# Kernel optimization log

Hardware: AMD Instinct MI355X
Metric: run time of the kernel (lower is better)

Reference implementation:

```python
import math
import jax, jax.numpy as jnp
import numpy as np

H = 8
DIM = 256
HD = DIM // H
SCALE = math.sqrt(HD)
EPS = 1e-16


def _segment_softmax(scores, dst, num_nodes):
    # scores: [E, H], dst: [E] -> softmax over edges sharing the same dst
    m = jax.ops.segment_max(scores, dst, num_segments=num_nodes)  # [N, H]
    m = jnp.where(jnp.isfinite(m), m, 0.0)  # empty segments -> -inf -> 0
    e = jnp.exp(scores - m[dst])
    s = jax.ops.segment_sum(e, dst, num_segments=num_nodes)  # [N, H]
    return e / (s[dst] + EPS)


def _graph_attention(x, edges, wq, bq, wk, bk, wv, bv, wo, bo):
    # x: [N, DIM]; edges: [2, E] (src, dst). Dropout is identity (eval mode).
    N = x.shape[0]
    Q = (x @ wq + bq).reshape(N, H, HD)
    K = (x @ wk + bk).reshape(N, H, HD)
    V = (x @ wv + bv).reshape(N, H, HD)
    src, dst = edges[0], edges[1]
    scores = jnp.einsum('ehd,ehd->eh', Q[dst], K[src]) / SCALE  # [E, H]
    attn = _segment_softmax(scores, dst, N)  # [E, H]
    msgs = V[src] * attn[:, :, None]  # [E, H, HD]
    out = jax.ops.segment_sum(msgs, dst, num_segments=N).reshape(N, DIM)
    return out @ wo + bo


def _linear_params(key, fan_in, fan_out):
    k1, k2 = jax.random.split(key)
    bound = 1.0 / math.sqrt(fan_in)
    w = jax.random.uniform(k1, (fan_in, fan_out), minval=-bound, maxval=bound, dtype=jnp.float32)
    b = jax.random.uniform(k2, (fan_out,), minval=-bound, maxval=bound, dtype=jnp.float32)
    return w, b


def setup_inputs() -> dict:
    key = jax.random.key(0)
    ks = jax.random.split(key, 12)
    n_slot, n_dom = 20000, 1000
    e_slot, e_dom = 320000, 16000
    inp = {
        'slot_x': jax.random.normal(ks[0], (n_slot, DIM), dtype=jnp.float32),
        'domain_x': jax.random.normal(ks[1], (n_dom, DIM), dtype=jnp.float32),
        'slot_edges': jax.random.randint(ks[2], (2, e_slot), 0, n_slot, dtype=jnp.int32),
        'domain_edges': jax.random.randint(ks[3], (2, e_dom), 0, n_dom, dtype=jnp.int32),
    }
    names = ['wq', 'wk', 'wv', 'wo']
    for i, nm in enumerate(names):
        w, b = _linear_params(ks[4 + i], DIM, DIM)
        inp[f'slot_{nm}'] = w
        inp[f'slot_{nm}_b'] = b
    for i, nm in enumerate(names):
        w, b = _linear_params(ks[8 + i], DIM, DIM)
        inp[f'dom_{nm}'] = w
        inp[f'dom_{nm}_b'] = b
    return inp


def reference(slot_x, domain_x, slot_edges, domain_edges,
              slot_wq, slot_wq_b, slot_wk, slot_wk_b, slot_wv, slot_wv_b, slot_wo, slot_wo_b,
              dom_wq, dom_wq_b, dom_wk, dom_wk_b, dom_wv, dom_wv_b, dom_wo, dom_wo_b):
    # slot branch: self-attention on slot graph + identity residual
    slot_out = _graph_attention(slot_x, slot_edges,
                                slot_wq, slot_wq_b, slot_wk, slot_wk_b,
                                slot_wv, slot_wv_b, slot_wo, slot_wo_b) + slot_x
    # domain branch
    dom_out = _graph_attention(domain_x, domain_edges,
                               dom_wq, dom_wq_b, dom_wk, dom_wk_b,
                               dom_wv, dom_wv_b, dom_wo, dom_wo_b) + domain_x
    return slot_out, dom_out
```

## Files before the change

### kernel.cpp

```cpp
#include <hip/hip_runtime.h>
#include <hip/hip_bf16.h>

#define DIM 256
#define INV_SCALE 0.17677669529663687f
#define SM_EPS 1e-16f
#define CAP 64
#define EPT 4

typedef unsigned short ushortT;
typedef unsigned int uintT;
typedef __attribute__((ext_vector_type(8))) __bf16 bf16x8;
typedef __attribute__((ext_vector_type(4))) float f32x4;

__device__ __forceinline__ float bf2f(ushortT u) {
    return __uint_as_float(((uintT)u) << 16);
}
__device__ __forceinline__ ushortT f2bf(float f) {
    uintT u = __float_as_uint(f);
    u += 0x7FFFu + ((u >> 16) & 1u);
    return (ushortT)(u >> 16);
}
template <int CTRL>
__device__ __forceinline__ float qperm_add(float p) {
    int v = __builtin_amdgcn_update_dpp(0, __float_as_int(p), CTRL, 0xF, 0xF, true);
    return p + __int_as_float(v);
}

struct WPack { const void* w[8]; const void* b[8]; };

__device__ __forceinline__ bool sniff_m16(const ushortT* __restrict__ x) {
    int lane = threadIdx.x & 63;
    ushortT u = x[lane * 2];
    int e = (u >> 7) & 0xFF;
    bool sane = ((u & 0x7FFFu) == 0) || (e >= 0x66 && e <= 0x90);
    unsigned long long m = __ballot(sane);
    return __popcll(m) >= 32;
}

__global__ __launch_bounds__(256) void megaA(
        const void* __restrict__ xs, const void* __restrict__ xd,
        const ushortT* __restrict__ sniff_src,
        ushortT* __restrict__ xb_s, ushortT* __restrict__ xb_d,
        WPack pk, ushortT* __restrict__ wT, float* __restrict__ biasF,
        int* __restrict__ flagWs,
        const int* __restrict__ src_s, const int* __restrict__ dst_s,
        const int* __restrict__ src_d, const int* __restrict__ dst_d,
        int* __restrict__ cnt_s, int* __restrict__ cnt_d,
        int* __restrict__ col_s, int* __restrict__ col_d,
        int Es_, int Ed_, int nSc,
        int n4s, int n4d, int nA0, int nA1)
{
    const int bid = blockIdx.x;
    const int t = threadIdx.x;

    if (bid < nSc) {
        const int base = bid * (256 * EPT) + t;
        #pragma unroll
        for (int u = 0; u < EPT; ++u) {
            const int idx = base + u * 256;
            if (idx < Es_) {
                const int dv = dst_s[idx];
                const int pos = atomicAdd(&cnt_s[dv], 1);
                if (pos < CAP) col_s[(dv << 6) + pos] = src_s[idx];
            } else {
                const int e = idx - Es_;
                if (e < Ed_) {
                    const int dv = dst_d[e];
                    const int pos = atomicAdd(&cnt_d[dv], 1);
                    if (pos < CAP) col_d[(dv << 6) + pos] = src_d[e];
                }
            }
        }
        return;
    }
    const bool m16 = sniff_m16(sniff_src);
    const int li2 = bid - nSc;

    if (li2 < nA0 + nA1) {
        const bool d = li2 >= nA0;
        const int li = d ? li2 - nA0 : li2;
        const int n4 = d ? n4d : n4s;
        const int i = li * 256 + t;
        if (i >= n4) return;
        const void* x = d ? xd : xs;
        ushortT* xb = d ? xb_d : xb_s;
        if (m16) {
            ((ushort4*)xb)[i] = ((const ushort4*)x)[i];
        } else {
            float4 v = ((const float4*)x)[i];
            ushort4 o2;
            o2.x = f2bf(v.x); o2.y = f2bf(v.y); o2.z = f2bf(v.z); o2.w = f2bf(v.w);
            ((ushort4*)xb)[i] = o2;
        }
    } else if (li2 < nA0 + nA1 + 128) {
        __shared__ float sh[64][65];
        const int r0 = li2 - (nA0 + nA1);
        const int which = r0 >> 4;
        const int tile = r0 & 15;
        const int tr = tile >> 2, tc = tile & 3;
        const void* w = pk.w[which];
        const int tx = t & 63, tg = t >> 6;
        #pragma unroll
        for (int i = 0; i < 16; ++i) {
            const int r = i * 4 + tg;
            const size_t si = (size_t)(tr * 64 + r) * 256 + tc * 64 + tx;
            sh[r][tx] = m16 ? bf2f(((const ushortT*)w)[si]) : ((const float*)w)[si];
        }
        __syncthreads();
        ushortT* o = wT + (size_t)which * 65536;
        #pragma unroll
        for (int i = 0; i < 16; ++i) {
            const int r = i * 4 + tg;
            o[(size_t)(tc * 64 + r) * 256 + tr * 64 + tx] = f2bf(sh[tx][r]);
        }
    } else if (li2 < nA0 + nA1 + 136) {
        const int which = li2 - (nA0 + nA1 + 128);
        const void* b = pk.b[which];
        float v = m16 ? bf2f(((const ushortT*)b)[t]) : ((const float*)b)[t];
        biasF[which * 256 + t] = v;
    } else {
        if (t == 0) *flagWs = m16 ? 1 : 0;
    }
}

__global__ __launch_bounds__(256, 2) void megaB(
        const ushortT* __restrict__ xb_s, const ushortT* __restrict__ xb_d,
        const ushortT* __restrict__ wT, const float* __restrict__ biasF,
        ushortT* __restrict__ q_s, ushortT* __restrict__ kv_s,
        ushortT* __restrict__ q_d, ushortT* __restrict__ kv_d,
        int Ms, int Md, int nbs_, int nbq_)
{
    const int bid = blockIdx.x;
    const int by  = bid / nbq_;
    const int bx0 = bid % nbq_;
    const bool dom = bx0 >= nbs_;
    const int bx = dom ? bx0 - nbs_ : bx0;
    const ushortT* A = dom ? xb_d : xb_s;
    const int M = dom ? Md : Ms;
    const int wbase = dom ? 4 : 0;
    ushortT* Q = dom ? q_d : q_s;
    ushortT* KV = dom ? kv_d : kv_s;

    __shared__ ushortT As[64 * 256];
    __shared__ ushortT Cs[3][64 * 70];

    const int tid  = threadIdx.x;
    const int wid  = tid >> 6;
    const int lane = tid & 63;
    const int m    = lane & 15;
    const int q    = lane >> 4;
    const int row0 = bx * 64;
    const int col0 = by * 64;
    const int colw = col0 + wid * 16 + m;

    {
        const int r  = tid >> 2;
        const int qt = tid & 3;
        const size_t rowAddr = (size_t)min(row0 + r, M - 1) * DIM;
        const int xr = r & 7;
        #pragma unroll
        for (int j = 0; j < 8; ++j) {
            const int chunk = qt * 8 + j;
            uint4 v = *(const uint4*)(A + rowAddr + chunk * 8);
            *(uint4*)&As[r * 256 + ((chunk ^ xr) * 8)] = v;
        }
    }

    const ushortT* Bp = wT + (size_t)wbase * 65536 + (size_t)colw * DIM + q * 8;
    bf16x8 bl[8][3];
    #pragma unroll
    for (int kk = 0; kk < 8; ++kk)
        #pragma unroll
        for (int z = 0; z < 3; ++z)
            bl[kk][z] = *(const bf16x8*)(Bp + (size_t)z * 65536 + kk * 32);

    f32x4 acc[3][4];
    #pragma unroll
    for (int z = 0; z < 3; ++z)
        #pragma unroll
        for (int i = 0; i < 4; ++i)
            acc[z][i] = (f32x4){0.f, 0.f, 0.f, 0.f};

    const int xm = m & 7;

    __syncthreads();

    #pragma unroll
    for (int kk = 0; kk < 8; ++kk) {
        bf16x8 af[4];
        #pragma unroll
        for (int i = 0; i < 4; ++i)
            af[i] = *(const bf16x8*)&As[(i * 16 + m) * 256 + (((q + 4 * kk) ^ xm) * 8)];
        #pragma unroll
        for (int z = 0; z < 3; ++z)
            #pragma unroll
            for (int i = 0; i < 4; ++i)
                acc[z][i] = __builtin_amdgcn_mfma_f32_16x16x32_bf16(bl[kk][z], af[i], acc[z][i], 0, 0, 0);
    }

    #pragma unroll
    for (int z = 0; z < 3; ++z) {
        const float4 b4 = *(const float4*)&biasF[(wbase + z) * 256 + col0 + wid * 16 + q * 4];
        #pragma unroll
        for (int i = 0; i < 4; ++i) {
            const int r = i * 16 + m;
            ushort4 o;
            o.x = f2bf(acc[z][i][0] + b4.x);
            o.y = f2bf(acc[z][i][1] + b4.y);
            o.z = f2bf(acc[z][i][2] + b4.z);
            o.w = f2bf(acc[z][i][3] + b4.w);
            *(ushort4*)&Cs[z][r * 70 + wid * 16 + q * 4] = o;
        }
    }
    __syncthreads();

    {
        const int r = tid >> 2;
        const int c = (tid & 3) * 16;
        const int row = row0 + r;
        if (row < M) {
            #pragma unroll
            for (int z = 0; z < 3; ++z) {
                uint4 v0 = *(const uint4*)&Cs[z][r * 70 + c];
                uint4 v1 = *(const uint4*)&Cs[z][r * 70 + c + 8];
                ushortT* C = (z == 0)
                    ? (Q + (size_t)row * DIM + col0 + c)
                    : (KV + (size_t)row * 512 + (z - 1) * 256 + col0 + c);
                *(uint4*)C = v0;
                *(uint4*)(C + 8) = v1;
            }
        }
    }
}

__global__ __launch_bounds__(256) void attn_kernel(
        const ushortT* __restrict__ Qs, const ushortT* __restrict__ KVs,
        const int* __restrict__ cnts, const int* __restrict__ css,
        ushortT* __restrict__ aggs,
        const ushortT* __restrict__ Qd_, const ushortT* __restrict__ KVd_,
        const int* __restrict__ cntd, const int* __restrict__ csd,
        ushortT* __restrict__ aggd,
        int Ns_, int Ntot)
{
    const int g = blockIdx.x * 4 + (threadIdx.x >> 6);
    if (g >= Ntot) return;
    const bool dom = g >= Ns_;
    const int d = dom ? g - Ns_ : g;
    const int t = threadIdx.x & 63;
    const ushortT* Qb = dom ? Qd_ : Qs;
    const ushortT* KVb = dom ? KVd_ : KVs;
    const int* cnt = dom ? cntd : cnts;
    const int* colsrc = dom ? csd : css;
    ushortT* aggb = dom ? aggd : aggs;

    const uintT t4 = (uintT)t * 4;
    const size_t cbase = (size_t)d * DIM + t4;
    uint2 qv = *(const uint2*)(Qb + cbase);
    const float q0 = bf2f((ushortT)(qv.x & 0xFFFF)), q1 = bf2f((ushortT)(qv.x >> 16));
    const float q2 = bf2f((ushortT)(qv.y & 0xFFFF)), q3 = bf2f((ushortT)(qv.y >> 16));

    float a0 = 0.f, a1 = 0.f, a2 = 0.f, a3 = 0.f, den = 0.f;

    auto PROC = [&](uint2 kvc, uint2 vvc) {
        float k0 = bf2f((ushortT)(kvc.x & 0xFFFF)), k1 = bf2f((ushortT)(kvc.x >> 16));
        float k2 = bf2f((ushortT)(kvc.y & 0xFFFF)), k3 = bf2f((ushortT)(kvc.y >> 16));
        float p = q0 * k0 + q1 * k1 + q2 * k2 + q3 * k3;
        p = qperm_add<0xB1>(p);
        p = qperm_add<0x4E>(p);
        p += __shfl_xor(p, 4, 8);
        const float w = __expf(fminf(p * INV_SCALE, 60.0f));
        den += w;
        a0 += w * bf2f((ushortT)(vvc.x & 0xFFFF));
        a1 += w * bf2f((ushortT)(vvc.x >> 16));
        a2 += w * bf2f((ushortT)(vvc.y & 0xFFFF));
        a3 += w * bf2f((ushortT)(vvc.y >> 16));
    };

    int deg = cnt[d];
    if (deg > CAP) deg = CAP;
    const int* cl = colsrc + ((size_t)d << 6);
    int i = 0;
    for (; i + 8 <= deg; i += 8) {
        const int4 c0 = *(const int4*)(cl + i);
        const int4 c1 = *(const int4*)(cl + i + 4);
        const uintT o0 = ((uintT)c0.x << 9) + t4;
        const uintT o1 = ((uintT)c0.y << 9) + t4;
        const uintT o2 = ((uintT)c0.z << 9) + t4;
        const uintT o3 = ((uintT)c0.w << 9) + t4;
        const uintT o4 = ((uintT)c1.x << 9) + t4;
        const uintT o5 = ((uintT)c1.y << 9) + t4;
        const uintT o6 = ((uintT)c1.z << 9) + t4;
        const uintT o7 = ((uintT)c1.w << 9) + t4;
        uint2 k0v = *(const uint2*)(KVb + o0), v0v = *(const uint2*)(KVb + o0 + 256);
        uint2 k1v = *(const uint2*)(KVb + o1), v1v = *(const uint2*)(KVb + o1 + 256);
        uint2 k2v = *(const uint2*)(KVb + o2), v2v = *(const uint2*)(KVb + o2 + 256);
        uint2 k3v = *(const uint2*)(KVb + o3), v3v = *(const uint2*)(KVb + o3 + 256);
        uint2 k4v = *(const uint2*)(KVb + o4), v4v = *(const uint2*)(KVb + o4 + 256);
        uint2 k5v = *(const uint2*)(KVb + o5), v5v = *(const uint2*)(KVb + o5 + 256);
        uint2 k6v = *(const uint2*)(KVb + o6), v6v = *(const uint2*)(KVb + o6 + 256);
        uint2 k7v = *(const uint2*)(KVb + o7), v7v = *(const uint2*)(KVb + o7 + 256);
        PROC(k0v, v0v); PROC(k1v, v1v); PROC(k2v, v2v); PROC(k3v, v3v);
        PROC(k4v, v4v); PROC(k5v, v5v); PROC(k6v, v6v); PROC(k7v, v7v);
    }
    for (; i + 4 <= deg; i += 4) {
        const int4 c0 = *(const int4*)(cl + i);
        const uintT o0 = ((uintT)c0.x << 9) + t4;
        const uintT o1 = ((uintT)c0.y << 9) + t4;
        const uintT o2 = ((uintT)c0.z << 9) + t4;
        const uintT o3 = ((uintT)c0.w << 9) + t4;
        uint2 k0v = *(const uint2*)(KVb + o0), v0v = *(const uint2*)(KVb + o0 + 256);
        uint2 k1v = *(const uint2*)(KVb + o1), v1v = *(const uint2*)(KVb + o1 + 256);
        uint2 k2v = *(const uint2*)(KVb + o2), v2v = *(const uint2*)(KVb + o2 + 256);
        uint2 k3v = *(const uint2*)(KVb + o3), v3v = *(const uint2*)(KVb + o3 + 256);
        PROC(k0v, v0v); PROC(k1v, v1v); PROC(k2v, v2v); PROC(k3v, v3v);
    }
    for (; i < deg; ++i) {
        const uintT sb = ((uintT)cl[i] << 9) + t4;
        uint2 kv = *(const uint2*)(KVb + sb);
        uint2 vv = *(const uint2*)(KVb + sb + 256);
        PROC(kv, vv);
    }

    const float r = 1.0f / (den + SM_EPS);
    ushort4 o;
    o.x = f2bf(a0 * r); o.y = f2bf(a1 * r); o.z = f2bf(a2 * r); o.w = f2bf(a3 * r);
    *(ushort4*)(aggb + cbase) = o;
}

__global__ __launch_bounds__(256, 2) void gemm_out(
        const ushortT* __restrict__ As_, const ushortT* __restrict__ Ad_,
        const ushortT* __restrict__ wT, const float* __restrict__ biasF,
        const void* __restrict__ xs, const void* __restrict__ xd,
        void* __restrict__ dout, int Ms, int Md, int nbs,
        const int* __restrict__ flag)
{
    const bool dom = (int)blockIdx.x >= nbs;
    const int bx = dom ? blockIdx.x - nbs : blockIdx.x;
    const ushortT* A = dom ? Ad_ : As_;
    const int M = dom ? Md : Ms;
    const int widx = 3 + (dom ? 4 : 0);
    const ushortT* BT = wT + (size_t)widx * 65536;
    const float* bias = biasF + widx * 256;
    const void* res = dom ? xd : xs;
    const size_t outOff = dom ? (size_t)Ms * DIM : 0;

    __shared__ ushortT As2[64 * 256];
    __shared__ float Cf[64 * 66];

    const int tid  = threadIdx.x;
    const int wid  = tid >> 6;
    const int lane = tid & 63;
    const int m    = lane & 15;
    const int q    = lane >> 4;
    const int row0 = bx * 64;
    const int col0 = blockIdx.y * 64;
    const int colw = col0 + wid * 16 + m;

    {
        const int r  = tid >> 2;
        const int qt = tid & 3;
        const size_t rowAddr = (size_t)min(row0 + r, M - 1) * DIM;
        const int xr = r & 7;
        #pragma unroll
        for (int j = 0; j < 8; ++j) {
            const int chunk = qt * 8 + j;
            uint4 v = *(const uint4*)(A + rowAddr + chunk * 8);
            *(uint4*)&As2[r * 256 + ((chunk ^ xr) * 8)] = v;
        }
    }

    const ushortT* Bp = BT + (size_t)colw * DIM + q * 8;
    bf16x8 bl[8];
    #pragma unroll
    for (int kk = 0; kk < 8; ++kk)
        bl[kk] = *(const bf16x8*)(Bp + kk * 32);

    f32x4 acc[4];
    #pragma unroll
    for (int i = 0; i < 4; ++i) acc[i] = (f32x4){0.f, 0.f, 0.f, 0.f};

    const int xm = m & 7;

    __syncthreads();

    #pragma unroll
    for (int kk = 0; kk < 8; ++kk) {
        bf16x8 af[4];
        #pragma unroll
        for (int i = 0; i < 4; ++i)
            af[i] = *(const bf16x8*)&As2[(i * 16 + m) * 256 + (((q + 4 * kk) ^ xm) * 8)];
        #pragma unroll
        for (int i = 0; i < 4; ++i)
            acc[i] = __builtin_amdgcn_mfma_f32_16x16x32_bf16(bl[kk], af[i], acc[i], 0, 0, 0);
    }

    {
        const float4 b4 = *(const float4*)&bias[col0 + wid * 16 + q * 4];
        #pragma unroll
        for (int i = 0; i < 4; ++i) {
            const int r = i * 16 + m;
            float4 o;
            o.x = acc[i][0] + b4.x;
            o.y = acc[i][1] + b4.y;
            o.z = acc[i][2] + b4.z;
            o.w = acc[i][3] + b4.w;
            *(float4*)&Cf[r * 66 + wid * 16 + q * 4] = o;
        }
    }
    __syncthreads();

    {
        const bool m16 = (*flag != 0);
        const int r = tid >> 2;
        const int c = (tid & 3) * 16;
        const int row = row0 + r;
        if (row < M) {
            const size_t ridx = (size_t)row * DIM + col0 + c;
            float v[16];
            #pragma unroll
            for (int j = 0; j < 16; j += 4) {
                float4 cv = *(const float4*)&Cf[r * 66 + c + j];
                v[j] = cv.x; v[j + 1] = cv.y; v[j + 2] = cv.z; v[j + 3] = cv.w;
            }
            if (m16) {
                const ushortT* rp = (const ushortT*)res + ridx;
                ushortT* op = (ushortT*)dout + outOff + ridx;
                uint4 r0 = *(const uint4*)rp;
                uint4 r1 = *(const uint4*)(rp + 8);
                ushortT tmp[16];
                const uintT* rw0 = (const uintT*)&r0;
                const uintT* rw1 = (const uintT*)&r1;
                #pragma unroll
                for (int j = 0; j < 4; ++j) {
                    tmp[2 * j]     = f2bf(v[2 * j]     + bf2f((ushortT)(rw0[j] & 0xFFFF)));
                    tmp[2 * j + 1] = f2bf(v[2 * j + 1] + bf2f((ushortT)(rw0[j] >> 16)));
                    tmp[8 + 2 * j]     = f2bf(v[8 + 2 * j]     + bf2f((ushortT)(rw1[j] & 0xFFFF)));
                    tmp[8 + 2 * j + 1] = f2bf(v[8 + 2 * j + 1] + bf2f((ushortT)(rw1[j] >> 16)));
                }
                *(uint4*)op = *(const uint4*)&tmp[0];
                *(uint4*)(op + 8) = *(const uint4*)&tmp[8];
            } else {
                const float* rp = (const float*)res + ridx;
                float* op = (float*)dout + outOff + ridx;
                #pragma unroll
                for (int j = 0; j < 16; j += 4) {
                    float4 rv = *(const float4*)(rp + j);
                    float4 o;
                    o.x = v[j] + rv.x; o.y = v[j + 1] + rv.y;
                    o.z = v[j + 2] + rv.z; o.w = v[j + 3] + rv.w;
                    *(float4*)(op + j) = o;
                }
            }
        }
    }
}

extern "C" void kernel_launch(void* const* d_in, const int* in_sizes, int n_in,
                              void* d_out, int out_size, void* d_ws, size_t ws_size,
                              hipStream_t stream)
{
    const void* slot_x = d_in[0];
    const void* dom_x  = d_in[1];
    const int* slot_edges = (const int*)d_in[2];
    const int* dom_edges  = (const int*)d_in[3];
    const int Ns = in_sizes[0] / DIM;
    const int Nd = in_sizes[1] / DIM;
    const int Es = in_sizes[2] / 2;
    const int Ed = in_sizes[3] / 2;

    WPack pk;
    for (int i = 0; i < 8; ++i) { pk.w[i] = d_in[4 + 2 * i]; pk.b[i] = d_in[5 + 2 * i]; }

    char* p = (char*)d_ws;
    size_t o = 0;
    auto take = [&](size_t b) { void* r = p + o; o = (o + b + 255) & ~(size_t)255; return r; };
    const size_t ndS = (size_t)Ns * DIM;
    const size_t ndD = (size_t)Nd * DIM;
    ushortT* xb_s  = (ushortT*)take(ndS * 2);
    ushortT* q_s   = (ushortT*)take(ndS * 2);
    ushortT* kv_s  = (ushortT*)take(2 * ndS * 2);
    ushortT* agg_s = (ushortT*)take(ndS * 2);
    ushortT* xb_d  = (ushortT*)take(ndD * 2);
    ushortT* q_d   = (ushortT*)take(ndD * 2);
    ushortT* kv_d  = (ushortT*)take(2 * ndD * 2);
    ushortT* agg_d = (ushortT*)take(ndD * 2);
    ushortT* wT    = (ushortT*)take(8 * 65536 * 2);
    float*   biasF = (float*)take(8 * 256 * 4);
    int* cnt_s = (int*)take((size_t)(Ns + Nd) * 4);
    int* cnt_d = cnt_s + Ns;
    int* col_s = (int*)take((size_t)Ns * CAP * 4);
    int* col_d = (int*)take((size_t)Nd * CAP * 4);
    int* flagWs = (int*)take(256);

    const int* src_s = slot_edges;
    const int* dst_s = slot_edges + Es;
    const int* src_d = dom_edges;
    const int* dst_d = dom_edges + Ed;

    const int n4s = Ns * DIM / 4, n4d = Nd * DIM / 4;
    const int nbs = (Ns + 63) / 64;
    const int nbd = (Nd + 63) / 64;
    const int nbq = nbs + nbd;

    (void)hipMemsetAsync(cnt_s, 0, (size_t)(Ns + Nd) * 4, stream);

    const int Etot = Es + Ed;
    const int nSc = (Etot + 256 * EPT - 1) / (256 * EPT);
    const int nA0 = (n4s + 255) / 256;
    const int nA1 = (n4d + 255) / 256;
    hipLaunchKernelGGL(megaA, dim3(nSc + nA0 + nA1 + 136 + 1), dim3(256), 0, stream,
                       slot_x, dom_x, (const ushortT*)slot_x, xb_s, xb_d,
                       pk, wT, biasF, flagWs,
                       src_s, dst_s, src_d, dst_d,
                       cnt_s, cnt_d, col_s, col_d,
                       Es, Ed, nSc, n4s, n4d, nA0, nA1);

    hipLaunchKernelGGL(megaB, dim3(nbq * 4), dim3(256), 0, stream,
                       xb_s, xb_d, wT, biasF, q_s, kv_s, q_d, kv_d,
                       Ns, Nd, nbs, nbq);

    const int Ntot = Ns + Nd;
    hipLaunchKernelGGL(attn_kernel, dim3((Ntot + 3) / 4), dim3(256), 0, stream,
                       q_s, kv_s, cnt_s, col_s, agg_s,
                       q_d, kv_d, cnt_d, col_d, agg_d,
                       Ns, Ntot);

    hipLaunchKernelGGL(gemm_out, dim3(nbq, DIM / 64), dim3(256), 0, stream,
                       agg_s, agg_d, wT, biasF, slot_x, dom_x, d_out,
                       Ns, Nd, nbs, flagWs);
}
```

Before: 222.1 us.

## Fuse x bf16 conversion into QKV GEMM and move edge scatter into it

Removes the separate pass that converts x to a bf16 staging buffer; the QKV GEMM now reads x directly and converts fp32 to bf16 while filling shared memory. Edge CSR scatter blocks move from the prep kernel into the GEMM kernel, so the prep kernel only transposes weights and biases. This saves a full read/write of x through the workspace and lets scatter overlap with the GEMM. The cost is that each GEMM column block re-reads fp32 x (four times as many blocks along columns), which doubles the load bytes per tile versus bf16.

```diff
diff --git a/kernel.cpp b/kernel.cpp
--- a/kernel.cpp
+++ b/kernel.cpp
@@ -38,23 +38,60 @@
 }
 
 __global__ __launch_bounds__(256) void megaA(
+        const ushortT* __restrict__ sniff_src,
+        WPack pk, ushortT* __restrict__ wT, float* __restrict__ biasF,
+        int* __restrict__ flagWs)
+{
+    const bool m16 = sniff_m16(sniff_src);
+    const int bid = blockIdx.x;
+    const int t = threadIdx.x;
+
+    if (bid < 128) {
+        __shared__ float sh[64][65];
+        const int which = bid >> 4;
+        const int tile = bid & 15;
+        const int tr = tile >> 2, tc = tile & 3;
+        const void* w = pk.w[which];
+        const int tx = t & 63, tg = t >> 6;
+        #pragma unroll
+        for (int i = 0; i < 16; ++i) {
+            const int r = i * 4 + tg;
+            const size_t si = (size_t)(tr * 64 + r) * 256 + tc * 64 + tx;
+            sh[r][tx] = m16 ? bf2f(((const ushortT*)w)[si]) : ((const float*)w)[si];
+        }
+        __syncthreads();
+        ushortT* o = wT + (size_t)which * 65536;
+        #pragma unroll
+        for (int i = 0; i < 16; ++i) {
+            const int r = i * 4 + tg;
+            o[(size_t)(tc * 64 + r) * 256 + tr * 64 + tx] = f2bf(sh[tx][r]);
+        }
+    } else if (bid < 136) {
+        const int which = bid - 128;
+        const void* b = pk.b[which];
+        float v = m16 ? bf2f(((const ushortT*)b)[t]) : ((const float*)b)[t];
+        biasF[which * 256 + t] = v;
+    } else {
+        if (t == 0) *flagWs = m16 ? 1 : 0;
+    }
+}
+
+__global__ __launch_bounds__(256, 2) void megaB(
         const void* __restrict__ xs, const void* __restrict__ xd,
         const ushortT* __restrict__ sniff_src,
-        ushortT* __restrict__ xb_s, ushortT* __restrict__ xb_d,
-        WPack pk, ushortT* __restrict__ wT, float* __restrict__ biasF,
-        int* __restrict__ flagWs,
+        const ushortT* __restrict__ wT, const float* __restrict__ biasF,
+        ushortT* __restrict__ q_s, ushortT* __restrict__ kv_s,
+        ushortT* __restrict__ q_d, ushortT* __restrict__ kv_d,
+        int Ms, int Md, int nbs_, int nbq_, int nSc,
         const int* __restrict__ src_s, const int* __restrict__ dst_s,
         const int* __restrict__ src_d, const int* __restrict__ dst_d,
         int* __restrict__ cnt_s, int* __restrict__ cnt_d,
         int* __restrict__ col_s, int* __restrict__ col_d,
-        int Es_, int Ed_, int nSc,
-        int n4s, int n4d, int nA0, int nA1)
+        int Es_, int Ed_)
 {
     const int bid = blockIdx.x;
-    const int t = threadIdx.x;
-
     if (bid < nSc) {
-        const int base = bid * (256 * EPT) + t;
+        const int base = bid * (256 * EPT) + threadIdx.x;
         #pragma unroll
         for (int u = 0; u < EPT; ++u) {
             const int idx = base + u * 256;
@@ -74,68 +111,12 @@
         return;
     }
     const bool m16 = sniff_m16(sniff_src);
-    const int li2 = bid - nSc;
-
-    if (li2 < nA0 + nA1) {
-        const bool d = li2 >= nA0;
-        const int li = d ? li2 - nA0 : li2;
-        const int n4 = d ? n4d : n4s;
-        const int i = li * 256 + t;
-        if (i >= n4) return;
-        const void* x = d ? xd : xs;
-        ushortT* xb = d ? xb_d : xb_s;
-        if (m16) {
-            ((ushort4*)xb)[i] = ((const ushort4*)x)[i];
-        } else {
-            float4 v = ((const float4*)x)[i];
-            ushort4 o2;
-            o2.x = f2bf(v.x); o2.y = f2bf(v.y); o2.z = f2bf(v.z); o2.w = f2bf(v.w);
-            ((ushort4*)xb)[i] = o2;
-        }
-    } else if (li2 < nA0 + nA1 + 128) {
-        __shared__ float sh[64][65];
-        const int r0 = li2 - (nA0 + nA1);
-        const int which = r0 >> 4;
-        const int tile = r0 & 15;
-        const int tr = tile >> 2, tc = tile & 3;
-        const void* w = pk.w[which];
-        const int tx = t & 63, tg = t >> 6;
-        #pragma unroll
-        for (int i = 0; i < 16; ++i) {
-            const int r = i * 4 + tg;
-            const size_t si = (size_t)(tr * 64 + r) * 256 + tc * 64 + tx;
-            sh[r][tx] = m16 ? bf2f(((const ushortT*)w)[si]) : ((const float*)w)[si];
-        }
-        __syncthreads();
-        ushortT* o = wT + (size_t)which * 65536;
-        #pragma unroll
-        for (int i = 0; i < 16; ++i) {
-            const int r = i * 4 + tg;
-            o[(size_t)(tc * 64 + r) * 256 + tr * 64 + tx] = f2bf(sh[tx][r]);
-        }
-    } else if (li2 < nA0 + nA1 + 136) {
-        const int which = li2 - (nA0 + nA1 + 128);
-        const void* b = pk.b[which];
-        float v = m16 ? bf2f(((const ushortT*)b)[t]) : ((const float*)b)[t];
-        biasF[which * 256 + t] = v;
-    } else {
-        if (t == 0) *flagWs = m16 ? 1 : 0;
-    }
-}
-
-__global__ __launch_bounds__(256, 2) void megaB(
-        const ushortT* __restrict__ xb_s, const ushortT* __restrict__ xb_d,
-        const ushortT* __restrict__ wT, const float* __restrict__ biasF,
-        ushortT* __restrict__ q_s, ushortT* __restrict__ kv_s,
-        ushortT* __restrict__ q_d, ushortT* __restrict__ kv_d,
-        int Ms, int Md, int nbs_, int nbq_)
-{
-    const int bid = blockIdx.x;
-    const int by  = bid / nbq_;
-    const int bx0 = bid % nbq_;
+    const int gbid = bid - nSc;
+    const int by  = gbid / nbq_;
+    const int bx0 = gbid % nbq_;
     const bool dom = bx0 >= nbs_;
     const int bx = dom ? bx0 - nbs_ : bx0;
-    const ushortT* A = dom ? xb_d : xb_s;
+    const void* X = dom ? xd : xs;
     const int M = dom ? Md : Ms;
     const int wbase = dom ? 4 : 0;
     ushortT* Q = dom ? q_d : q_s;
@@ -156,13 +137,30 @@
     {
         const int r  = tid >> 2;
         const int qt = tid & 3;
-        const size_t rowAddr = (size_t)min(row0 + r, M - 1) * DIM;
         const int xr = r & 7;
-        #pragma unroll
-        for (int j = 0; j < 8; ++j) {
-            const int chunk = qt * 8 + j;
-            uint4 v = *(const uint4*)(A + rowAddr + chunk * 8);
-            *(uint4*)&As[r * 256 + ((chunk ^ xr) * 8)] = v;
+        const int row = min(row0 + r, M - 1);
+        if (m16) {
+            const ushortT* src = (const ushortT*)X + (size_t)row * DIM;
+            #pragma unroll
+            for (int j = 0; j < 8; ++j) {
+                const int chunk = qt * 8 + j;
+                uint4 v = *(const uint4*)(src + chunk * 8);
+                *(uint4*)&As[r * 256 + ((chunk ^ xr) * 8)] = v;
+            }
+        } else {
+            const float* src = (const float*)X + (size_t)row * DIM;
+            #pragma unroll
+            for (int j = 0; j < 8; ++j) {
+                const int chunk = qt * 8 + j;
+                float4 f0 = *(const float4*)(src + chunk * 8);
+                float4 f1 = *(const float4*)(src + chunk * 8 + 4);
+                ushort4 a, b;
+                a.x = f2bf(f0.x); a.y = f2bf(f0.y); a.z = f2bf(f0.z); a.w = f2bf(f0.w);
+                b.x = f2bf(f1.x); b.y = f2bf(f1.y); b.z = f2bf(f1.z); b.w = f2bf(f1.w);
+                ushortT* d = &As[r * 256 + ((chunk ^ xr) * 8)];
+                *(ushort4*)d = a;
+                *(ushort4*)(d + 4) = b;
+            }
         }
     }
 
@@ -476,11 +474,9 @@
     auto take = [&](size_t b) { void* r = p + o; o = (o + b + 255) & ~(size_t)255; return r; };
     const size_t ndS = (size_t)Ns * DIM;
     const size_t ndD = (size_t)Nd * DIM;
-    ushortT* xb_s  = (ushortT*)take(ndS * 2);
     ushortT* q_s   = (ushortT*)take(ndS * 2);
     ushortT* kv_s  = (ushortT*)take(2 * ndS * 2);
     ushortT* agg_s = (ushortT*)take(ndS * 2);
-    ushortT* xb_d  = (ushortT*)take(ndD * 2);
     ushortT* q_d   = (ushortT*)take(ndD * 2);
     ushortT* kv_d  = (ushortT*)take(2 * ndD * 2);
     ushortT* agg_d = (ushortT*)take(ndD * 2);
@@ -497,27 +493,23 @@
     const int* src_d = dom_edges;
     const int* dst_d = dom_edges + Ed;
 
-    const int n4s = Ns * DIM / 4, n4d = Nd * DIM / 4;
     const int nbs = (Ns + 63) / 64;
     const int nbd = (Nd + 63) / 64;
     const int nbq = nbs + nbd;
 
     (void)hipMemsetAsync(cnt_s, 0, (size_t)(Ns + Nd) * 4, stream);
 
+    hipLaunchKernelGGL(megaA, dim3(137), dim3(256), 0, stream,
+                       (const ushortT*)slot_x, pk, wT, biasF, flagWs);
+
     const int Etot = Es + Ed;
     const int nSc = (Etot + 256 * EPT - 1) / (256 * EPT);
-    const int nA0 = (n4s + 255) / 256;
-    const int nA1 = (n4d + 255) / 256;
-    hipLaunchKernelGGL(megaA, dim3(nSc + nA0 + nA1 + 136 + 1), dim3(256), 0, stream,
-                       slot_x, dom_x, (const ushortT*)slot_x, xb_s, xb_d,
-                       pk, wT, biasF, flagWs,
+    hipLaunchKernelGGL(megaB, dim3(nSc + nbq * 4), dim3(256), 0, stream,
+                       slot_x, dom_x, (const ushortT*)slot_x, wT, biasF,
+                       q_s, kv_s, q_d, kv_d,
+                       Ns, Nd, nbs, nbq, nSc,
                        src_s, dst_s, src_d, dst_d,
-                       cnt_s, cnt_d, col_s, col_d,
-                       Es, Ed, nSc, n4s, n4d, nA0, nA1);
-
-    hipLaunchKernelGGL(megaB, dim3(nbq * 4), dim3(256), 0, stream,
-                       xb_s, xb_d, wT, biasF, q_s, kv_s, q_d, kv_d,
-                       Ns, Nd, nbs, nbq);
+                       cnt_s, cnt_d, col_s, col_d, Es, Ed);
 
     const int Ntot = Ns + Nd;
     hipLaunchKernelGGL(attn_kernel, dim3((Ntot + 3) / 4), dim3(256), 0, stream,
```

Result: no change. 221.8 us (-0.1%).
